# Kernel tuning notes

Measured on AMD Instinct MI355X. Metric: run time of the kernel, lower is better.

## Reference

```python
import jax, jax.numpy as jnp
import numpy as np

N_EMBD = 768
N_HEAD = 8
HEAD_DIM = N_EMBD // N_HEAD


def setup_inputs() -> dict:
    key = jax.random.key(0)
    k1, k2, k3 = jax.random.split(key, 3)
    B, T, C = 8, 1024, N_EMBD
    x = jax.random.normal(k1, (B, T, C), dtype=jnp.float32)
    # nn.Linear(C, 3C, bias=False): store as [C, 3C] so y = x @ W
    W_attn = jax.random.normal(k2, (C, 3 * C), dtype=jnp.float32) * (1.0 / np.sqrt(C))
    W_proj = jax.random.normal(k3, (C, C), dtype=jnp.float32) * (1.0 / np.sqrt(C))
    return {"x": x, "W_attn": W_attn, "W_proj": W_proj}


def reference(x, W_attn, W_proj):
    B, T, C = x.shape
    qkv = x @ W_attn                      # [B,T,3C]
    q, k, v = jnp.split(qkv, 3, axis=2)
    # [B,T,C] -> [B,H,T,D]
    def heads(t):
        return t.reshape(B, T, N_HEAD, HEAD_DIM).transpose(0, 2, 1, 3)
    q, k, v = heads(q), heads(k), heads(v)
    scale = 1.0 / np.sqrt(HEAD_DIM)
    att = jnp.einsum('bhtd,bhsd->bhts', q, k) * scale  # [B,H,T,T]
    causal = jnp.tril(jnp.ones((T, T), dtype=bool))
    att = jnp.where(causal[None, None], att, -jnp.inf)
    att = jax.nn.softmax(att, axis=-1)
    y = jnp.einsum('bhts,bhsd->bhtd', att, v)          # [B,H,T,D]
    y = y.transpose(0, 2, 1, 3).reshape(B, T, C)
    return y @ W_proj
```

## Files before the change

### kernel.cpp

```cpp
#include <hip/hip_runtime.h>
#include <stdint.h>

#define Bz 8
#define Tz 1024
#define Cz 768
#define Hz 8
#define Dz 96
#define BHz 64
#define Kz 768

typedef __bf16 bf16x8 __attribute__((ext_vector_type(8)));
typedef unsigned short u16x8 __attribute__((ext_vector_type(8)));
typedef float f32x4 __attribute__((ext_vector_type(4)));

__device__ __forceinline__ unsigned short f2bf(float f) {
  union { float f; unsigned int u; } v; v.f = f;
  unsigned int u = v.u;
  return (unsigned short)((u + 0x7fffu + ((u >> 16) & 1u)) >> 16);
}

typedef const __attribute__((address_space(1))) void* gas_ptr;
typedef __attribute__((address_space(3))) void* las_ptr;
__device__ __forceinline__ void gl16(const void* g, void* l) {
  __builtin_amdgcn_global_load_lds((gas_ptr)g, (las_ptr)l, 16, 0, 0);
}

__global__ __launch_bounds__(256) void cast_f32_bf16(const float* __restrict__ in,
                                                     unsigned short* __restrict__ out) {
  int i = (blockIdx.x * 256 + threadIdx.x) * 4;
  float4 v = *(const float4*)(in + i);
  union { unsigned short s[4]; uint2 u; } o;
  o.s[0] = f2bf(v.x); o.s[1] = f2bf(v.y); o.s[2] = f2bf(v.z); o.s[3] = f2bf(v.w);
  *(uint2*)(out + i) = o.u;
}

__global__ __launch_bounds__(256) void transpose_cast(const float* __restrict__ in,
                                                      unsigned short* __restrict__ out,
                                                      int R, int Cc) {
  __shared__ unsigned short t[64][72];
  int bx = blockIdx.x * 64;
  int by = blockIdx.y * 64;
  int tid = threadIdx.x;
#pragma unroll
  for (int i = 0; i < 16; i++) {
    int idx = tid + i * 256;
    int r = idx >> 6, c = idx & 63;
    t[c][r] = f2bf(in[(by + r) * Cc + bx + c]);
  }
  __syncthreads();
#pragma unroll
  for (int i = 0; i < 16; i++) {
    int idx = tid + i * 256;
    int r = idx >> 6, c = idx & 63;
    out[(bx + r) * R + by + c] = t[r][c];
  }
}

template <int MODE>
__global__ __launch_bounds__(256)
void gemm128(const unsigned short* __restrict__ A,
             const unsigned short* __restrict__ Bt,
             unsigned short* __restrict__ obf,
             float* __restrict__ of32) {
  __shared__ unsigned short Asm[128 * 32];
  __shared__ unsigned short Bsm[128 * 32];
  const int tid = threadIdx.x;
  const int wave = tid >> 6, lane = tid & 63;
  const int quad = lane >> 4, l16 = lane & 15;
  const int bm = blockIdx.x, bn = blockIdx.y;
  const int wm = (wave >> 1) * 64, wn = (wave & 1) * 64;

  f32x4 zero = {0.f, 0.f, 0.f, 0.f};
  f32x4 acc[4][4];
#pragma unroll
  for (int i = 0; i < 4; i++)
#pragma unroll
    for (int j = 0; j < 4; j++) acc[i][j] = zero;

  const int rr = lane >> 2, c8 = (lane & 3) * 8;
  const unsigned short* Ag0 = A + (size_t)(bm * 128 + wave * 32 + rr) * Kz + c8;
  const unsigned short* Ag1 = Ag0 + 16 * Kz;
  const unsigned short* Bg0 = Bt + (size_t)(bn * 128 + wave * 32 + rr) * Kz + c8;
  const unsigned short* Bg1 = Bg0 + 16 * Kz;
  unsigned short* lA0 = &Asm[wave * 1024];
  unsigned short* lA1 = lA0 + 512;
  unsigned short* lB0 = &Bsm[wave * 1024];
  unsigned short* lB1 = lB0 + 512;

  for (int k0 = 0; k0 < Kz; k0 += 32) {
    __syncthreads();
    gl16(Ag0 + k0, lA0);
    gl16(Ag1 + k0, lA1);
    gl16(Bg0 + k0, lB0);
    gl16(Bg1 + k0, lB1);
    __syncthreads();
    bf16x8 af[4], bfr[4];
#pragma unroll
    for (int mi = 0; mi < 4; mi++)
      af[mi] = *(const bf16x8*)&Asm[(wm + mi * 16 + l16) * 32 + quad * 8];
#pragma unroll
    for (int ni = 0; ni < 4; ni++)
      bfr[ni] = *(const bf16x8*)&Bsm[(wn + ni * 16 + l16) * 32 + quad * 8];
#pragma unroll
    for (int mi = 0; mi < 4; mi++)
#pragma unroll
      for (int ni = 0; ni < 4; ni++)
        acc[mi][ni] = __builtin_amdgcn_mfma_f32_16x16x32_bf16(af[mi], bfr[ni], acc[mi][ni], 0, 0, 0);
  }

#pragma unroll
  for (int mi = 0; mi < 4; mi++) {
    int row = bm * 128 + wm + mi * 16 + quad * 4;
    if (MODE == 0) {
      int b = row >> 10;
      int t = row & 1023;
#pragma unroll
      for (int ni = 0; ni < 4; ni++) {
        int col = bn * 128 + wn + ni * 16 + l16;
        int which = col / 768;
        int cc = col - which * 768;
        int h = cc / 96;
        int d = cc - h * 96;
        int base = ((which * 64 + b * 8 + h) * 1024 + t) * 96 + d;
#pragma unroll
        for (int r = 0; r < 4; r++) obf[base + r * 96] = f2bf(acc[mi][ni][r]);
      }
    } else {
#pragma unroll
      for (int ni = 0; ni < 4; ni++) {
        int col = bn * 128 + wn + ni * 16 + l16;
#pragma unroll
        for (int r = 0; r < 4; r++) of32[(row + r) * 768 + col] = acc[mi][ni][r];
      }
    }
  }
}

__global__ __launch_bounds__(256, 2)
void attn(const unsigned short* __restrict__ qkv, unsigned short* __restrict__ y) {
  const int bh = blockIdx.x;
  const int q0 = (7 - blockIdx.y) * 128;
  const int tid = threadIdx.x;
  const int wave = tid >> 6, lane = tid & 63;
  const int quad = lane >> 4, l16 = lane & 15;
  const int qw0 = q0 + wave * 32;
  const int b = bh >> 3, h = bh & 7;

  const unsigned short* Qh = qkv + bh * Tz * Dz;
  const unsigned short* Kh = qkv + (BHz + bh) * Tz * Dz;
  const unsigned short* Vh = qkv + (2 * BHz + bh) * Tz * Dz;

  __shared__ unsigned short Vsm[96 * 136];
  __shared__ unsigned short Psm[4 * 32 * 136];
  unsigned short* Pw = Psm + wave * 32 * 136;

  bf16x8 aq[2][3];
#pragma unroll
  for (int mi = 0; mi < 2; mi++)
#pragma unroll
    for (int kd = 0; kd < 3; kd++)
      aq[mi][kd] = *(const bf16x8*)(Qh + (qw0 + mi * 16 + l16) * Dz + kd * 32 + quad * 8);

  f32x4 zero = {0.f, 0.f, 0.f, 0.f};
  f32x4 acc_o[2][6];
#pragma unroll
  for (int mi = 0; mi < 2; mi++)
#pragma unroll
    for (int i = 0; i < 6; i++) acc_o[mi][i] = zero;
  const float NEG = -__builtin_inff();
  float mrow[2][4], lrow[2][4];
#pragma unroll
  for (int mi = 0; mi < 2; mi++)
#pragma unroll
    for (int r = 0; r < 4; r++) { mrow[mi][r] = NEG; lrow[mi][r] = 0.f; }
  const float scale = 0.10206207261596577f;

  const int sg = tid & 127;
  const int g0 = tid >> 7;
  const unsigned short* Vrow = Vh + sg * Dz;

  for (int s0 = 0; s0 <= q0; s0 += 128) {
    __syncthreads();
#pragma unroll
    for (int i = 0; i < 6; i++) {
      int g = g0 + 2 * i;
      u16x8 v = *(const u16x8*)(Vrow + s0 * Dz + g * 8);
#pragma unroll
      for (int jj = 0; jj < 8; jj++) Vsm[(g * 8 + jj) * 136 + sg] = v[jj];
    }
    __syncthreads();

    const int srem = qw0 + 31 - s0;
    const int nlim = min(7, srem >> 4);
    const int klim = min(3, srem >> 5);

    f32x4 sacc[2][8];
#pragma unroll
    for (int ni = 0; ni < 8; ni++) {
      if (ni <= nlim) {
        sacc[0][ni] = zero; sacc[1][ni] = zero;
#pragma unroll
        for (int kd = 0; kd < 3; kd++) {
          bf16x8 bk = *(const bf16x8*)(Kh + (s0 + ni * 16 + l16) * Dz + kd * 32 + quad * 8);
          sacc[0][ni] = __builtin_amdgcn_mfma_f32_16x16x32_bf16(aq[0][kd], bk, sacc[0][ni], 0, 0, 0);
          sacc[1][ni] = __builtin_amdgcn_mfma_f32_16x16x32_bf16(aq[1][kd], bk, sacc[1][ni], 0, 0, 0);
        }
      }
    }

#pragma unroll
    for (int mi = 0; mi < 2; mi++) {
      float rmax[4] = {NEG, NEG, NEG, NEG};
#pragma unroll
      for (int ni = 0; ni < 8; ni++) {
        if (ni <= nlim) {
#pragma unroll
          for (int r = 0; r < 4; r++) {
            int t_abs = qw0 + mi * 16 + quad * 4 + r;
            int s_abs = s0 + ni * 16 + l16;
            float v = (s_abs > t_abs) ? NEG : sacc[mi][ni][r] * scale;
            sacc[mi][ni][r] = v;
            rmax[r] = fmaxf(rmax[r], v);
          }
        }
      }
#pragma unroll
      for (int r = 0; r < 4; r++)
#pragma unroll
        for (int sh = 1; sh < 16; sh <<= 1)
          rmax[r] = fmaxf(rmax[r], __shfl_xor(rmax[r], sh));

      float alpha[4], rsum[4];
#pragma unroll
      for (int r = 0; r < 4; r++) {
        float mnew = fmaxf(mrow[mi][r], rmax[r]);
        alpha[r] = __expf(mrow[mi][r] - mnew);
        mrow[mi][r] = mnew;
        rsum[r] = 0.f;
      }
#pragma unroll
      for (int ni = 0; ni < 8; ni++) {
        if (ni <= nlim) {
#pragma unroll
          for (int r = 0; r < 4; r++) {
            float p = __expf(sacc[mi][ni][r] - mrow[mi][r]);
            rsum[r] += p;
            Pw[(mi * 16 + quad * 4 + r) * 136 + ni * 16 + l16] = f2bf(p);
          }
        }
      }
#pragma unroll
      for (int r = 0; r < 4; r++) {
#pragma unroll
        for (int sh = 1; sh < 16; sh <<= 1) rsum[r] += __shfl_xor(rsum[r], sh);
        lrow[mi][r] = lrow[mi][r] * alpha[r] + rsum[r];
      }
#pragma unroll
      for (int di = 0; di < 6; di++)
#pragma unroll
        for (int r = 0; r < 4; r++) acc_o[mi][di][r] *= alpha[r];
    }

#pragma unroll
    for (int kc = 0; kc < 4; kc++) {
      if (kc <= klim) {
        bf16x8 ap0 = *(const bf16x8*)&Pw[l16 * 136 + kc * 32 + quad * 8];
        bf16x8 ap1 = *(const bf16x8*)&Pw[(16 + l16) * 136 + kc * 32 + quad * 8];
#pragma unroll
        for (int di = 0; di < 6; di++) {
          bf16x8 bv = *(const bf16x8*)&Vsm[(di * 16 + l16) * 136 + kc * 32 + quad * 8];
          acc_o[0][di] = __builtin_amdgcn_mfma_f32_16x16x32_bf16(ap0, bv, acc_o[0][di], 0, 0, 0);
          acc_o[1][di] = __builtin_amdgcn_mfma_f32_16x16x32_bf16(ap1, bv, acc_o[1][di], 0, 0, 0);
        }
      }
    }
  }

#pragma unroll
  for (int mi = 0; mi < 2; mi++) {
#pragma unroll
    for (int r = 0; r < 4; r++) {
      float linv = 1.f / lrow[mi][r];
      int t = qw0 + mi * 16 + quad * 4 + r;
#pragma unroll
      for (int di = 0; di < 6; di++) {
        int d = di * 16 + l16;
        y[(b * Tz + t) * Cz + h * Dz + d] = f2bf(acc_o[mi][di][r] * linv);
      }
    }
  }
}

#define OFF_XB   0u
#define OFF_WAT  12582912u
#define OFF_WPT  16121856u
#define OFF_QKV  17301504u
#define OFF_Y    55050240u

extern "C" void kernel_launch(void* const* d_in, const int* in_sizes, int n_in,
                              void* d_out, int out_size, void* d_ws, size_t ws_size,
                              hipStream_t stream) {
  const float* x  = (const float*)d_in[0];
  const float* Wa = (const float*)d_in[1];
  const float* Wp = (const float*)d_in[2];
  float* out = (float*)d_out;
  uint8_t* ws = (uint8_t*)d_ws;
  unsigned short* xb  = (unsigned short*)(ws + OFF_XB);
  unsigned short* Wat = (unsigned short*)(ws + OFF_WAT);
  unsigned short* Wpt = (unsigned short*)(ws + OFF_WPT);
  unsigned short* qkv = (unsigned short*)(ws + OFF_QKV);
  unsigned short* y   = (unsigned short*)(ws + OFF_Y);

  cast_f32_bf16<<<6144, 256, 0, stream>>>(x, xb);
  transpose_cast<<<dim3(36, 12), 256, 0, stream>>>(Wa, Wat, 768, 2304);
  transpose_cast<<<dim3(12, 12), 256, 0, stream>>>(Wp, Wpt, 768, 768);
  gemm128<0><<<dim3(64, 18), 256, 0, stream>>>(xb, Wat, qkv, nullptr);
  attn<<<dim3(64, 8), 256, 0, stream>>>(qkv, y);
  gemm128<1><<<dim3(64, 6), 256, 0, stream>>>(y, Wpt, nullptr, out);
}
```

Measured before the change: 214.4 us.

## Keep attention probabilities in registers via transposed S and 16x16x16 MFMA

The attention kernel now computes S transposed (K as the A operand), so each lane holds one query row. That lets the softmax probabilities be packed straight into bf16 registers as the B operand of 16x16x16 MFMAs for P·V, which removes the per-wave P shared-memory buffer and its write/read round trip. Row reductions shrink to two cross-lane shuffles, a finer causal limit skips MFMAs for the first 16-row sub-tile, V tiles are prefetched into registers one iteration ahead, and output stores are vectorized. Occupancy hint is raised to 3 blocks per SM; the risks are more register pressure and the less efficient K=16 MFMA shape for P·V.

```diff
diff --git a/kernel.cpp b/kernel.cpp
--- a/kernel.cpp
+++ b/kernel.cpp
@@ -12,11 +12,19 @@
 typedef __bf16 bf16x8 __attribute__((ext_vector_type(8)));
 typedef unsigned short u16x8 __attribute__((ext_vector_type(8)));
 typedef float f32x4 __attribute__((ext_vector_type(4)));
+typedef short s16x4 __attribute__((ext_vector_type(4)));
 
 __device__ __forceinline__ unsigned short f2bf(float f) {
   union { float f; unsigned int u; } v; v.f = f;
   unsigned int u = v.u;
   return (unsigned short)((u + 0x7fffu + ((u >> 16) & 1u)) >> 16);
+}
+
+__device__ __forceinline__ s16x4 pack4(f32x4 p) {
+  s16x4 o;
+  o[0] = (short)f2bf(p[0]); o[1] = (short)f2bf(p[1]);
+  o[2] = (short)f2bf(p[2]); o[3] = (short)f2bf(p[3]);
+  return o;
 }
 
 typedef const __attribute__((address_space(1))) void* gas_ptr;
@@ -136,7 +144,7 @@
   }
 }
 
-__global__ __launch_bounds__(256, 2)
+__global__ __launch_bounds__(256, 3)
 void attn(const unsigned short* __restrict__ qkv, unsigned short* __restrict__ y) {
   const int bh = blockIdx.x;
   const int q0 = (7 - blockIdx.y) * 128;
@@ -151,8 +159,6 @@
   const unsigned short* Vh = qkv + (2 * BHz + bh) * Tz * Dz;
 
   __shared__ unsigned short Vsm[96 * 136];
-  __shared__ unsigned short Psm[4 * 32 * 136];
-  unsigned short* Pw = Psm + wave * 32 * 136;
 
   bf16x8 aq[2][3];
 #pragma unroll
@@ -168,109 +174,105 @@
 #pragma unroll
     for (int i = 0; i < 6; i++) acc_o[mi][i] = zero;
   const float NEG = -__builtin_inff();
-  float mrow[2][4], lrow[2][4];
-#pragma unroll
-  for (int mi = 0; mi < 2; mi++)
-#pragma unroll
-    for (int r = 0; r < 4; r++) { mrow[mi][r] = NEG; lrow[mi][r] = 0.f; }
+  float mrow[2] = {NEG, NEG}, lrow[2] = {0.f, 0.f};
   const float scale = 0.10206207261596577f;
 
   const int sg = tid & 127;
   const int g0 = tid >> 7;
   const unsigned short* Vrow = Vh + sg * Dz;
+  u16x8 vpref[6];
+#pragma unroll
+  for (int i = 0; i < 6; i++)
+    vpref[i] = *(const u16x8*)(Vrow + (g0 + 2 * i) * 8);
 
   for (int s0 = 0; s0 <= q0; s0 += 128) {
     __syncthreads();
 #pragma unroll
     for (int i = 0; i < 6; i++) {
       int g = g0 + 2 * i;
-      u16x8 v = *(const u16x8*)(Vrow + s0 * Dz + g * 8);
-#pragma unroll
-      for (int jj = 0; jj < 8; jj++) Vsm[(g * 8 + jj) * 136 + sg] = v[jj];
+#pragma unroll
+      for (int jj = 0; jj < 8; jj++) Vsm[(g * 8 + jj) * 136 + sg] = vpref[i][jj];
     }
     __syncthreads();
-
-    const int srem = qw0 + 31 - s0;
-    const int nlim = min(7, srem >> 4);
-    const int klim = min(3, srem >> 5);
+    if (s0 + 128 <= q0) {
+#pragma unroll
+      for (int i = 0; i < 6; i++)
+        vpref[i] = *(const u16x8*)(Vrow + (s0 + 128) * Dz + (g0 + 2 * i) * 8);
+    }
+
+    const int nlim0 = min(7, (qw0 + 15 - s0) >> 4);
+    const int nlim1 = min(7, (qw0 + 31 - s0) >> 4);
 
     f32x4 sacc[2][8];
 #pragma unroll
     for (int ni = 0; ni < 8; ni++) {
-      if (ni <= nlim) {
-        sacc[0][ni] = zero; sacc[1][ni] = zero;
+      if (ni <= nlim1) {
+        sacc[1][ni] = zero;
+        if (ni <= nlim0) sacc[0][ni] = zero;
 #pragma unroll
         for (int kd = 0; kd < 3; kd++) {
-          bf16x8 bk = *(const bf16x8*)(Kh + (s0 + ni * 16 + l16) * Dz + kd * 32 + quad * 8);
-          sacc[0][ni] = __builtin_amdgcn_mfma_f32_16x16x32_bf16(aq[0][kd], bk, sacc[0][ni], 0, 0, 0);
-          sacc[1][ni] = __builtin_amdgcn_mfma_f32_16x16x32_bf16(aq[1][kd], bk, sacc[1][ni], 0, 0, 0);
+          bf16x8 ak = *(const bf16x8*)(Kh + (s0 + ni * 16 + l16) * Dz + kd * 32 + quad * 8);
+          sacc[1][ni] = __builtin_amdgcn_mfma_f32_16x16x32_bf16(ak, aq[1][kd], sacc[1][ni], 0, 0, 0);
+          if (ni <= nlim0)
+            sacc[0][ni] = __builtin_amdgcn_mfma_f32_16x16x32_bf16(ak, aq[0][kd], sacc[0][ni], 0, 0, 0);
         }
       }
     }
 
+    s16x4 pk[2][8];
 #pragma unroll
     for (int mi = 0; mi < 2; mi++) {
-      float rmax[4] = {NEG, NEG, NEG, NEG};
+      const int nl = mi ? nlim1 : nlim0;
+      const int t_abs = qw0 + mi * 16 + l16;
+      float rmax = NEG;
 #pragma unroll
       for (int ni = 0; ni < 8; ni++) {
-        if (ni <= nlim) {
+        if (ni <= nl) {
 #pragma unroll
           for (int r = 0; r < 4; r++) {
-            int t_abs = qw0 + mi * 16 + quad * 4 + r;
-            int s_abs = s0 + ni * 16 + l16;
+            int s_abs = s0 + ni * 16 + quad * 4 + r;
             float v = (s_abs > t_abs) ? NEG : sacc[mi][ni][r] * scale;
             sacc[mi][ni][r] = v;
-            rmax[r] = fmaxf(rmax[r], v);
+            rmax = fmaxf(rmax, v);
           }
         }
       }
-#pragma unroll
-      for (int r = 0; r < 4; r++)
-#pragma unroll
-        for (int sh = 1; sh < 16; sh <<= 1)
-          rmax[r] = fmaxf(rmax[r], __shfl_xor(rmax[r], sh));
-
-      float alpha[4], rsum[4];
-#pragma unroll
-      for (int r = 0; r < 4; r++) {
-        float mnew = fmaxf(mrow[mi][r], rmax[r]);
-        alpha[r] = __expf(mrow[mi][r] - mnew);
-        mrow[mi][r] = mnew;
-        rsum[r] = 0.f;
-      }
+      rmax = fmaxf(rmax, __shfl_xor(rmax, 16));
+      rmax = fmaxf(rmax, __shfl_xor(rmax, 32));
+      float mnew = fmaxf(mrow[mi], rmax);
+      float alpha = __expf(mrow[mi] - mnew);
+      mrow[mi] = mnew;
+      float rsum = 0.f;
 #pragma unroll
       for (int ni = 0; ni < 8; ni++) {
-        if (ni <= nlim) {
+        if (ni <= nl) {
+          f32x4 p;
 #pragma unroll
           for (int r = 0; r < 4; r++) {
-            float p = __expf(sacc[mi][ni][r] - mrow[mi][r]);
-            rsum[r] += p;
-            Pw[(mi * 16 + quad * 4 + r) * 136 + ni * 16 + l16] = f2bf(p);
+            p[r] = __expf(sacc[mi][ni][r] - mnew);
+            rsum += p[r];
           }
+          pk[mi][ni] = pack4(p);
         }
       }
-#pragma unroll
-      for (int r = 0; r < 4; r++) {
-#pragma unroll
-        for (int sh = 1; sh < 16; sh <<= 1) rsum[r] += __shfl_xor(rsum[r], sh);
-        lrow[mi][r] = lrow[mi][r] * alpha[r] + rsum[r];
-      }
+      rsum += __shfl_xor(rsum, 16);
+      rsum += __shfl_xor(rsum, 32);
+      lrow[mi] = lrow[mi] * alpha + rsum;
 #pragma unroll
       for (int di = 0; di < 6; di++)
 #pragma unroll
-        for (int r = 0; r < 4; r++) acc_o[mi][di][r] *= alpha[r];
-    }
-
-#pragma unroll
-    for (int kc = 0; kc < 4; kc++) {
-      if (kc <= klim) {
-        bf16x8 ap0 = *(const bf16x8*)&Pw[l16 * 136 + kc * 32 + quad * 8];
-        bf16x8 ap1 = *(const bf16x8*)&Pw[(16 + l16) * 136 + kc * 32 + quad * 8];
+        for (int r = 0; r < 4; r++) acc_o[mi][di][r] *= alpha;
+    }
+
+#pragma unroll
+    for (int ni = 0; ni < 8; ni++) {
+      if (ni <= nlim1) {
 #pragma unroll
         for (int di = 0; di < 6; di++) {
-          bf16x8 bv = *(const bf16x8*)&Vsm[(di * 16 + l16) * 136 + kc * 32 + quad * 8];
-          acc_o[0][di] = __builtin_amdgcn_mfma_f32_16x16x32_bf16(ap0, bv, acc_o[0][di], 0, 0, 0);
-          acc_o[1][di] = __builtin_amdgcn_mfma_f32_16x16x32_bf16(ap1, bv, acc_o[1][di], 0, 0, 0);
+          s16x4 av = *(const s16x4*)&Vsm[(di * 16 + l16) * 136 + ni * 16 + quad * 4];
+          acc_o[1][di] = __builtin_amdgcn_mfma_f32_16x16x16bf16_1k(av, pk[1][ni], acc_o[1][di], 0, 0, 0);
+          if (ni <= nlim0)
+            acc_o[0][di] = __builtin_amdgcn_mfma_f32_16x16x16bf16_1k(av, pk[0][ni], acc_o[0][di], 0, 0, 0);
         }
       }
     }
@@ -278,15 +280,15 @@
 
 #pragma unroll
   for (int mi = 0; mi < 2; mi++) {
-#pragma unroll
-    for (int r = 0; r < 4; r++) {
-      float linv = 1.f / lrow[mi][r];
-      int t = qw0 + mi * 16 + quad * 4 + r;
-#pragma unroll
-      for (int di = 0; di < 6; di++) {
-        int d = di * 16 + l16;
-        y[(b * Tz + t) * Cz + h * Dz + d] = f2bf(acc_o[mi][di][r] * linv);
-      }
+    float linv = 1.f / lrow[mi];
+    int t = qw0 + mi * 16 + l16;
+#pragma unroll
+    for (int di = 0; di < 6; di++) {
+      union { unsigned short s[4]; uint2 u; } o;
+#pragma unroll
+      for (int r = 0; r < 4; r++) o.s[r] = f2bf(acc_o[mi][di][r] * linv);
+      int d = di * 16 + quad * 4;
+      *(uint2*)&y[(size_t)(b * Tz + t) * Cz + h * Dz + d] = o.u;
     }
   }
 }
```

After: 449.1 us. 2.09x slower.
